# Performance work log

Measured on AMD Instinct MI355X. Metric: run time of the kernel, lower is better.

The kernel has to match this reference:

```python
import jax, jax.numpy as jnp
import numpy as np

HEADS = 16
HEAD_DIM = 128


def rotate_half(x):
    x1, x2 = x[..., : x.shape[-1] // 2], x[..., x.shape[-1] // 2 :]
    return jnp.concatenate((-x2, x1), axis=-1)


def setup_inputs() -> dict:
    key = jax.random.key(0)
    ks = jax.random.split(key, 8)
    b, s, h = 2, 2048, 2048
    d = HEAD_DIM
    sc = 1.0 / np.sqrt(h)
    x = jax.random.normal(ks[0], (b, s, h), jnp.float32)
    # real RoPE angles for realism
    inv_freq = 1.0 / (10000.0 ** (jnp.arange(0, d, 2, dtype=jnp.float32) / d))
    t = jnp.arange(s, dtype=jnp.float32)
    freqs = jnp.outer(t, inv_freq)  # [s, d/2]
    emb = jnp.concatenate((freqs, freqs), axis=-1)  # [s, d]
    return {
        "x": x,
        "cos": jnp.cos(emb),
        "sin": jnp.sin(emb),
        "wq": jax.random.normal(ks[1], (h, h), jnp.float32) * sc,
        "bq": jnp.zeros((h,), jnp.float32),
        "wk": jax.random.normal(ks[2], (h, h), jnp.float32) * sc,
        "bk": jnp.zeros((h,), jnp.float32),
        "wv": jax.random.normal(ks[3], (h, h), jnp.float32) * sc,
        "bv": jnp.zeros((h,), jnp.float32),
        "wo": jax.random.normal(ks[4], (h, h), jnp.float32) * sc,
    }


def reference(x, cos, sin, wq, bq, wk, bk, wv, bv, wo):
    b, s, hidden = x.shape
    nh, d = HEADS, HEAD_DIM
    # QKV projections (F.linear: x @ W.T + b)
    def split_heads(t):
        return t.reshape(b, s, nh, d).transpose(0, 2, 1, 3)  # [b,h,s,d]
    q = split_heads(x @ wq.T + bq)
    k = split_heads(x @ wk.T + bk)
    v = split_heads(x @ wv.T + bv)
    # RoPE (cos/sin: [s,d] broadcast over [b,h,s,d])
    q = q * cos + rotate_half(q) * sin
    k = k * cos + rotate_half(k) * sin
    # full (non-causal) attention, materializing [b,h,s,s] scores as original
    scale = 1.0 / jnp.sqrt(jnp.asarray(d, x.dtype))
    scores = jnp.einsum("bhqd,bhkd->bhqk", q, k) * scale
    attn = jax.nn.softmax(scores, axis=-1)
    out = jnp.einsum("bhqk,bhkd->bhqd", attn, v)  # [b,h,s,d]
    out = out.transpose(0, 2, 1, 3).reshape(b, s, hidden)
    # o_proj: no bias
    return out @ wo.T
```

## Files before the change

kernel.cpp:

```cpp
#include <hip/hip_runtime.h>

#define B_  2
#define NH  16
#define S_  2048
#define D_  128
#define HID 2048

typedef _Float16 half_t;
typedef _Float16 f16x8 __attribute__((ext_vector_type(8)));
typedef _Float16 f16x4_t __attribute__((ext_vector_type(4)));
typedef float f32x4 __attribute__((ext_vector_type(4)));

__device__ __forceinline__ void glds16(const half_t* g, half_t* l) {
    __builtin_amdgcn_global_load_lds(
        (const __attribute__((address_space(1))) void*)g,
        (__attribute__((address_space(3))) void*)l, 16, 0, 0);
}
__device__ __forceinline__ float fexp2(float x) { return __builtin_amdgcn_exp2f(x); }

__global__ __launch_bounds__(256) void cvt_all(
    const float* __restrict__ x,  const float* __restrict__ wq, const float* __restrict__ wk,
    const float* __restrict__ wv, const float* __restrict__ wo, half_t* __restrict__ dst)
{
    long i = ((long)blockIdx.x * 256 + threadIdx.x) * 4;
    const float* src; long off;
    if (i < 8388608)       { src = x;  off = i; }
    else if (i < 12582912) { src = wq; off = i - 8388608; }
    else if (i < 16777216) { src = wk; off = i - 12582912; }
    else if (i < 20971520) { src = wv; off = i - 16777216; }
    else                   { src = wo; off = i - 20971520; }
    float4 v = *(const float4*)(src + off);
    f16x4_t h;
    h[0] = (half_t)v.x; h[1] = (half_t)v.y; h[2] = (half_t)v.z; h[3] = (half_t)v.w;
    *(f16x4_t*)(dst + i) = h;
}

__global__ __launch_bounds__(256, 3) void qkv_gemm(
    const half_t* __restrict__ xb,
    const half_t* __restrict__ wqb, const half_t* __restrict__ wkb, const half_t* __restrict__ wvb,
    const float* __restrict__ bq, const float* __restrict__ bk, const float* __restrict__ bv,
    const float* __restrict__ cosp, const float* __restrict__ sinp,
    half_t* __restrict__ qo, half_t* __restrict__ ko, half_t* __restrict__ vto)
{
    __shared__ __align__(16) half_t As[128 * 32];
    __shared__ __align__(16) half_t Bs[128 * 32];
    const int m0 = blockIdx.x * 128;
    const int n0 = blockIdx.y * 128;
    const int z  = blockIdx.z;
    const half_t* wb   = (z == 0) ? wqb : (z == 1) ? wkb : wvb;
    const float*  bias = (z == 0) ? bq  : (z == 1) ? bk  : bv;
    const int tid = threadIdx.x, wave = tid >> 6, lane = tid & 63;
    const int quad = lane >> 4, lrow = lane & 15;
    const int wm = wave >> 1, wn = wave & 1;

    const int r0 = wave * 32 + (lane >> 2);
    const int r1 = r0 + 16;
    const int c0 = (((lane & 3) - (r0 >> 1)) & 3) * 8;
    const int c1 = (((lane & 3) - (r1 >> 1)) & 3) * 8;
    const half_t* ag0 = xb + (size_t)(m0 + r0) * HID + c0;
    const half_t* ag1 = xb + (size_t)(m0 + r1) * HID + c1;
    const half_t* bg0 = wb + (size_t)(n0 + r0) * HID + c0;
    const half_t* bg1 = wb + (size_t)(n0 + r1) * HID + c1;
    half_t* al0 = &As[(wave * 32) * 32];
    half_t* al1 = &As[(wave * 32 + 16) * 32];
    half_t* bl0 = &Bs[(wave * 32) * 32];
    half_t* bl1 = &Bs[(wave * 32 + 16) * 32];

    f32x4 acc[4][4] = {};

    for (int k0 = 0; k0 < HID; k0 += 32) {
        __syncthreads();
        glds16(ag0 + k0, al0);
        glds16(ag1 + k0, al1);
        glds16(bg0 + k0, bl0);
        glds16(bg1 + k0, bl1);
        __syncthreads();
        f16x8 af[4], bf[4];
#pragma unroll
        for (int mt = 0; mt < 4; mt++) {
            const int ra = wm * 64 + mt * 16 + lrow;
            const int pa = (quad + (ra >> 1)) & 3;
            af[mt] = *(const f16x8*)&As[ra * 32 + pa * 8];
        }
#pragma unroll
        for (int nt = 0; nt < 4; nt++) {
            const int rb = wn * 16 + nt * 32 + lrow;
            const int pb = (quad + (rb >> 1)) & 3;
            bf[nt] = *(const f16x8*)&Bs[rb * 32 + pb * 8];
        }
#pragma unroll
        for (int mt = 0; mt < 4; mt++)
#pragma unroll
            for (int nt = 0; nt < 4; nt++)
                acc[mt][nt] = __builtin_amdgcn_mfma_f32_16x16x32_f16(af[mt], bf[nt], acc[mt][nt], 0, 0, 0);
    }

    const int head = blockIdx.y;
    float bs_[4];
#pragma unroll
    for (int nt = 0; nt < 4; nt++) bs_[nt] = bias[n0 + nt * 32 + wn * 16 + lrow];
#pragma unroll
    for (int mt = 0; mt < 4; mt++) {
#pragma unroll
        for (int r = 0; r < 4; r++) {
            const int m  = m0 + wm * 64 + mt * 16 + quad * 4 + r;
            const int bb = m >> 11;
            const int st = m & (S_ - 1);
            float res[4];
#pragma unroll
            for (int nt = 0; nt < 4; nt++) res[nt] = acc[mt][nt][r] + bs_[nt];
            if (z < 2) {
                const float* cr = cosp + st * D_;
                const float* sr = sinp + st * D_;
#pragma unroll
                for (int pr = 0; pr < 2; pr++) {
                    const int dlo = pr * 32 + wn * 16 + lrow;
                    float cl = cr[dlo], sl = sr[dlo], ch = cr[dlo + 64], sh = sr[dlo + 64];
                    float lo = res[pr], hi = res[pr + 2];
                    res[pr]     = lo * cl - hi * sl;
                    res[pr + 2] = hi * ch + lo * sh;
                }
                half_t* dst = (z == 0 ? qo : ko) + ((size_t)(bb * NH + head) * S_ + st) * D_;
#pragma unroll
                for (int nt = 0; nt < 4; nt++) dst[nt * 32 + wn * 16 + lrow] = (half_t)res[nt];
            } else {
                half_t* dst = vto + (size_t)(bb * NH + head) * D_ * S_ + st;
#pragma unroll
                for (int nt = 0; nt < 4; nt++) dst[(size_t)(nt * 32 + wn * 16 + lrow) * S_] = (half_t)res[nt];
            }
        }
    }
}

#define PLD 72
__global__ __launch_bounds__(256, 2) void attn_kernel(
    const half_t* __restrict__ qb, const half_t* __restrict__ kb,
    const half_t* __restrict__ vtb, half_t* __restrict__ ob)
{
    __shared__ __align__(16) half_t ks[64 * 128];
    __shared__ __align__(16) half_t vs[128 * 64];
    __shared__ __align__(16) half_t ps[4 * 32 * PLD];
    const int head = blockIdx.y, b = blockIdx.z;
    const int bh = b * NH + head;
    const int tid = threadIdx.x, wave = tid >> 6, lane = tid & 63;
    const int quad = lane >> 4, lrow = lane & 15;
    const float SC = 0.08838834764831845f * 1.4426950408889634f;
    const int q0 = blockIdx.x * 128 + wave * 32;

    f16x8 qf[2][4];
#pragma unroll
    for (int mt = 0; mt < 2; mt++) {
        const half_t* qrow = qb + ((size_t)bh * S_ + q0 + mt * 16 + lrow) * D_;
#pragma unroll
        for (int kc = 0; kc < 4; kc++) {
            f16x8 v = *(const f16x8*)(qrow + kc * 32 + quad * 8);
#pragma unroll
            for (int j = 0; j < 8; j++) v[j] = (half_t)((float)v[j] * SC);
            qf[mt][kc] = v;
        }
    }

    const half_t* kbase = kb + (size_t)bh * S_ * D_;
    const half_t* vbase = vtb + (size_t)bh * D_ * S_;
    const int pbase = wave * 32 * PLD;

    float m_run[2] = {-1e30f, -1e30f}, l_run[2] = {0.f, 0.f};
    f32x4 o[2][8] = {};

    for (int kt = 0; kt < 32; kt++) {
        __syncthreads();
#pragma unroll
        for (int i = 0; i < 4; i++) {
            const int rk = wave * 16 + i * 4 + (lane >> 4);
            const int ck = (((lane & 15) - (rk & 7)) & 15) * 8;
            glds16(kbase + (size_t)(kt * 64 + rk) * D_ + ck, &ks[(wave * 16 + i * 4) * 128]);
            const int rv = wave * 32 + i * 8 + (lane >> 3);
            const int cv = (((lane & 7) - (rv & 7)) & 7) * 8;
            glds16(vbase + (size_t)rv * S_ + kt * 64 + cv, &vs[(wave * 32 + i * 8) * 64]);
        }
        __syncthreads();

        f32x4 st[2][4] = {};
#pragma unroll
        for (int nt = 0; nt < 4; nt++) {
            const int rk2 = nt * 16 + lrow;
#pragma unroll
            for (int kc = 0; kc < 4; kc++) {
                const int pk = (kc * 4 + quad + (rk2 & 7)) & 15;
                f16x8 kf = *(const f16x8*)&ks[rk2 * 128 + pk * 8];
                st[0][nt] = __builtin_amdgcn_mfma_f32_16x16x32_f16(kf, qf[0][kc], st[0][nt], 0, 0, 0);
                st[1][nt] = __builtin_amdgcn_mfma_f32_16x16x32_f16(kf, qf[1][kc], st[1][nt], 0, 0, 0);
            }
        }

        bool upd = false;
        float alpha[2];
#pragma unroll
        for (int mt = 0; mt < 2; mt++) {
            float m01 = fmaxf(fmaxf(st[mt][0][0], st[mt][0][1]), fmaxf(st[mt][0][2], st[mt][0][3]));
            float m11 = fmaxf(fmaxf(st[mt][1][0], st[mt][1][1]), fmaxf(st[mt][1][2], st[mt][1][3]));
            float m21 = fmaxf(fmaxf(st[mt][2][0], st[mt][2][1]), fmaxf(st[mt][2][2], st[mt][2][3]));
            float m31 = fmaxf(fmaxf(st[mt][3][0], st[mt][3][1]), fmaxf(st[mt][3][2], st[mt][3][3]));
            float mx = fmaxf(fmaxf(m01, m11), fmaxf(m21, m31));
            mx = fmaxf(mx, __shfl_xor(mx, 16));
            mx = fmaxf(mx, __shfl_xor(mx, 32));
            const float mnew = fmaxf(m_run[mt], mx);
            alpha[mt] = fexp2(m_run[mt] - mnew);
            upd = upd || (mnew > m_run[mt]);
            m_run[mt] = mnew;
            float rs = 0.f;
#pragma unroll
            for (int nt = 0; nt < 4; nt++) {
                f16x4_t pk4;
#pragma unroll
                for (int r = 0; r < 4; r++) {
                    float p = fexp2(st[mt][nt][r] - mnew);
                    rs += p;
                    pk4[r] = (half_t)p;
                }
                *(f16x4_t*)&ps[pbase + (mt * 16 + lrow) * PLD + nt * 16 + quad * 4] = pk4;
            }
            rs += __shfl_xor(rs, 16);
            rs += __shfl_xor(rs, 32);
            l_run[mt] = l_run[mt] * alpha[mt] + rs;
        }
        if (__any(upd)) {
#pragma unroll
            for (int mt = 0; mt < 2; mt++) {
                float ab[4];
#pragma unroll
                for (int r = 0; r < 4; r++) ab[r] = __shfl(alpha[mt], quad * 4 + r, 16);
#pragma unroll
                for (int dt = 0; dt < 8; dt++)
#pragma unroll
                    for (int r = 0; r < 4; r++) o[mt][dt][r] *= ab[r];
            }
        }

#pragma unroll
        for (int kc2 = 0; kc2 < 2; kc2++) {
            f16x8 pf0 = *(const f16x8*)&ps[pbase + lrow * PLD + kc2 * 32 + quad * 8];
            f16x8 pf1 = *(const f16x8*)&ps[pbase + (16 + lrow) * PLD + kc2 * 32 + quad * 8];
#pragma unroll
            for (int dt = 0; dt < 8; dt++) {
                const int rv2 = dt * 16 + lrow;
                const int pv = (kc2 * 4 + quad + (rv2 & 7)) & 7;
                f16x8 vf = *(const f16x8*)&vs[rv2 * 64 + pv * 8];
                o[0][dt] = __builtin_amdgcn_mfma_f32_16x16x32_f16(pf0, vf, o[0][dt], 0, 0, 0);
                o[1][dt] = __builtin_amdgcn_mfma_f32_16x16x32_f16(pf1, vf, o[1][dt], 0, 0, 0);
            }
        }
    }

#pragma unroll
    for (int mt = 0; mt < 2; mt++) {
        const float rl = 1.f / l_run[mt];
        float rb[4];
#pragma unroll
        for (int r = 0; r < 4; r++) rb[r] = __shfl(rl, quad * 4 + r, 16);
#pragma unroll
        for (int dt = 0; dt < 8; dt++) {
            const int d = dt * 16 + lrow;
#pragma unroll
            for (int r = 0; r < 4; r++) {
                const int row = q0 + mt * 16 + quad * 4 + r;
                ob[((size_t)b * S_ + row) * HID + head * D_ + d] = (half_t)(o[mt][dt][r] * rb[r]);
            }
        }
    }
}

__global__ __launch_bounds__(256, 3) void out_gemm(
    const half_t* __restrict__ ab, const half_t* __restrict__ wob, float* __restrict__ out)
{
    __shared__ __align__(16) half_t As[128 * 32];
    __shared__ __align__(16) half_t Bs[128 * 32];
    const int m0 = blockIdx.x * 128;
    const int n0 = blockIdx.y * 128;
    const int tid = threadIdx.x, wave = tid >> 6, lane = tid & 63;
    const int quad = lane >> 4, lrow = lane & 15;
    const int wm = wave >> 1, wn = wave & 1;

    const int r0 = wave * 32 + (lane >> 2);
    const int r1 = r0 + 16;
    const int c0 = (((lane & 3) - (r0 >> 1)) & 3) * 8;
    const int c1 = (((lane & 3) - (r1 >> 1)) & 3) * 8;
    const half_t* ag0 = ab  + (size_t)(m0 + r0) * HID + c0;
    const half_t* ag1 = ab  + (size_t)(m0 + r1) * HID + c1;
    const half_t* bg0 = wob + (size_t)(n0 + r0) * HID + c0;
    const half_t* bg1 = wob + (size_t)(n0 + r1) * HID + c1;
    half_t* al0 = &As[(wave * 32) * 32];
    half_t* al1 = &As[(wave * 32 + 16) * 32];
    half_t* bl0 = &Bs[(wave * 32) * 32];
    half_t* bl1 = &Bs[(wave * 32 + 16) * 32];

    f32x4 acc[4][4] = {};

    for (int k0 = 0; k0 < HID; k0 += 32) {
        __syncthreads();
        glds16(ag0 + k0, al0);
        glds16(ag1 + k0, al1);
        glds16(bg0 + k0, bl0);
        glds16(bg1 + k0, bl1);
        __syncthreads();
        f16x8 af[4], bf[4];
#pragma unroll
        for (int mt = 0; mt < 4; mt++) {
            const int ra = wm * 64 + mt * 16 + lrow;
            const int pa = (quad + (ra >> 1)) & 3;
            af[mt] = *(const f16x8*)&As[ra * 32 + pa * 8];
        }
#pragma unroll
        for (int nt = 0; nt < 4; nt++) {
            const int rb = wn * 16 + nt * 32 + lrow;
            const int pb = (quad + (rb >> 1)) & 3;
            bf[nt] = *(const f16x8*)&Bs[rb * 32 + pb * 8];
        }
#pragma unroll
        for (int mt = 0; mt < 4; mt++)
#pragma unroll
            for (int nt = 0; nt < 4; nt++)
                acc[mt][nt] = __builtin_amdgcn_mfma_f32_16x16x32_f16(af[mt], bf[nt], acc[mt][nt], 0, 0, 0);
    }

#pragma unroll
    for (int mt = 0; mt < 4; mt++)
#pragma unroll
        for (int r = 0; r < 4; r++) {
            const int m = m0 + wm * 64 + mt * 16 + quad * 4 + r;
#pragma unroll
            for (int nt = 0; nt < 4; nt++)
                out[(size_t)m * HID + n0 + nt * 32 + wn * 16 + lrow] = acc[mt][nt][r];
        }
}

extern "C" void kernel_launch(void* const* d_in, const int* in_sizes, int n_in,
                              void* d_out, int out_size, void* d_ws, size_t ws_size,
                              hipStream_t stream)
{
    const float* x    = (const float*)d_in[0];
    const float* cosp = (const float*)d_in[1];
    const float* sinp = (const float*)d_in[2];
    const float* wq   = (const float*)d_in[3];
    const float* bq   = (const float*)d_in[4];
    const float* wk   = (const float*)d_in[5];
    const float* bk   = (const float*)d_in[6];
    const float* wv   = (const float*)d_in[7];
    const float* bv   = (const float*)d_in[8];
    const float* wo   = (const float*)d_in[9];
    float* out = (float*)d_out;

    half_t* w   = (half_t*)d_ws;
    half_t* xb  = w;
    half_t* wqb = xb  + 8388608;
    half_t* wkb = wqb + 4194304;
    half_t* wvb = wkb + 4194304;
    half_t* wob = wvb + 4194304;
    half_t* qo  = wob + 4194304;
    half_t* ko  = qo  + 8388608;
    half_t* vto = ko  + 8388608;
    half_t* ob  = vto + 8388608;

    cvt_all<<<24576, 256, 0, stream>>>(x, wq, wk, wv, wo, xb);
    qkv_gemm<<<dim3(32, 16, 3), 256, 0, stream>>>(xb, wqb, wkb, wvb, bq, bk, bv,
                                                  cosp, sinp, qo, ko, vto);
    attn_kernel<<<dim3(16, 16, 2), 256, 0, stream>>>(qo, ko, vto, ob);
    out_gemm<<<dim3(32, 16), 256, 0, stream>>>(ob, wob, out);
}
```

Before: 422.4 us.

## Load GEMM and attention operands directly from global memory, dropping LDS staging

Removes the shared-memory staging (global_load_lds plus barriers) in the QKV GEMM, output GEMM and attention kernels. Each wave now loads its MFMA fragments straight from global memory into registers. The GEMMs double-buffer those register fragments to prefetch the next k-slice. The aim is to cut barrier and LDS traffic, but every wave now re-reads operands from global/L2 that were previously shared across the block, which raises memory traffic and register pressure.

```diff
diff --git a/kernel.cpp b/kernel.cpp
--- a/kernel.cpp
+++ b/kernel.cpp
@@ -11,11 +11,6 @@
 typedef _Float16 f16x4_t __attribute__((ext_vector_type(4)));
 typedef float f32x4 __attribute__((ext_vector_type(4)));
 
-__device__ __forceinline__ void glds16(const half_t* g, half_t* l) {
-    __builtin_amdgcn_global_load_lds(
-        (const __attribute__((address_space(1))) void*)g,
-        (__attribute__((address_space(3))) void*)l, 16, 0, 0);
-}
 __device__ __forceinline__ float fexp2(float x) { return __builtin_amdgcn_exp2f(x); }
 
 __global__ __launch_bounds__(256) void cvt_all(
@@ -42,8 +37,6 @@
     const float* __restrict__ cosp, const float* __restrict__ sinp,
     half_t* __restrict__ qo, half_t* __restrict__ ko, half_t* __restrict__ vto)
 {
-    __shared__ __align__(16) half_t As[128 * 32];
-    __shared__ __align__(16) half_t Bs[128 * 32];
     const int m0 = blockIdx.x * 128;
     const int n0 = blockIdx.y * 128;
     const int z  = blockIdx.z;
@@ -53,47 +46,37 @@
     const int quad = lane >> 4, lrow = lane & 15;
     const int wm = wave >> 1, wn = wave & 1;
 
-    const int r0 = wave * 32 + (lane >> 2);
-    const int r1 = r0 + 16;
-    const int c0 = (((lane & 3) - (r0 >> 1)) & 3) * 8;
-    const int c1 = (((lane & 3) - (r1 >> 1)) & 3) * 8;
-    const half_t* ag0 = xb + (size_t)(m0 + r0) * HID + c0;
-    const half_t* ag1 = xb + (size_t)(m0 + r1) * HID + c1;
-    const half_t* bg0 = wb + (size_t)(n0 + r0) * HID + c0;
-    const half_t* bg1 = wb + (size_t)(n0 + r1) * HID + c1;
-    half_t* al0 = &As[(wave * 32) * 32];
-    half_t* al1 = &As[(wave * 32 + 16) * 32];
-    half_t* bl0 = &Bs[(wave * 32) * 32];
-    half_t* bl1 = &Bs[(wave * 32 + 16) * 32];
-
+    const half_t* ap = xb + (size_t)(m0 + wm * 64 + lrow) * HID + quad * 8;
+    const half_t* bp = wb + (size_t)(n0 + wn * 16 + lrow) * HID + quad * 8;
+
+    f16x8 afr[2][4], bfr[2][4];
     f32x4 acc[4][4] = {};
 
-    for (int k0 = 0; k0 < HID; k0 += 32) {
-        __syncthreads();
-        glds16(ag0 + k0, al0);
-        glds16(ag1 + k0, al1);
-        glds16(bg0 + k0, bl0);
-        glds16(bg1 + k0, bl1);
-        __syncthreads();
-        f16x8 af[4], bf[4];
-#pragma unroll
-        for (int mt = 0; mt < 4; mt++) {
-            const int ra = wm * 64 + mt * 16 + lrow;
-            const int pa = (quad + (ra >> 1)) & 3;
-            af[mt] = *(const f16x8*)&As[ra * 32 + pa * 8];
-        }
-#pragma unroll
-        for (int nt = 0; nt < 4; nt++) {
-            const int rb = wn * 16 + nt * 32 + lrow;
-            const int pb = (quad + (rb >> 1)) & 3;
-            bf[nt] = *(const f16x8*)&Bs[rb * 32 + pb * 8];
-        }
+#pragma unroll
+    for (int mt = 0; mt < 4; mt++) afr[0][mt] = *(const f16x8*)(ap + (size_t)mt * 16 * HID);
+#pragma unroll
+    for (int nt = 0; nt < 4; nt++) bfr[0][nt] = *(const f16x8*)(bp + (size_t)nt * 32 * HID);
+
+#pragma unroll 2
+    for (int k0 = 0; k0 < HID - 32; k0 += 32) {
+        const int p = (k0 >> 5) & 1, pn = p ^ 1;
 #pragma unroll
         for (int mt = 0; mt < 4; mt++)
+            afr[pn][mt] = *(const f16x8*)(ap + k0 + 32 + (size_t)mt * 16 * HID);
+#pragma unroll
+        for (int nt = 0; nt < 4; nt++)
+            bfr[pn][nt] = *(const f16x8*)(bp + k0 + 32 + (size_t)nt * 32 * HID);
+#pragma unroll
+        for (int mt = 0; mt < 4; mt++)
 #pragma unroll
             for (int nt = 0; nt < 4; nt++)
-                acc[mt][nt] = __builtin_amdgcn_mfma_f32_16x16x32_f16(af[mt], bf[nt], acc[mt][nt], 0, 0, 0);
-    }
+                acc[mt][nt] = __builtin_amdgcn_mfma_f32_16x16x32_f16(afr[p][mt], bfr[p][nt], acc[mt][nt], 0, 0, 0);
+    }
+#pragma unroll
+    for (int mt = 0; mt < 4; mt++)
+#pragma unroll
+        for (int nt = 0; nt < 4; nt++)
+            acc[mt][nt] = __builtin_amdgcn_mfma_f32_16x16x32_f16(afr[1][mt], bfr[1][nt], acc[mt][nt], 0, 0, 0);
 
     const int head = blockIdx.y;
     float bs_[4];
@@ -137,8 +120,6 @@
     const half_t* __restrict__ qb, const half_t* __restrict__ kb,
     const half_t* __restrict__ vtb, half_t* __restrict__ ob)
 {
-    __shared__ __align__(16) half_t ks[64 * 128];
-    __shared__ __align__(16) half_t vs[128 * 64];
     __shared__ __align__(16) half_t ps[4 * 32 * PLD];
     const int head = blockIdx.y, b = blockIdx.z;
     const int bh = b * NH + head;
@@ -168,28 +149,17 @@
     f32x4 o[2][8] = {};
 
     for (int kt = 0; kt < 32; kt++) {
-        __syncthreads();
-#pragma unroll
-        for (int i = 0; i < 4; i++) {
-            const int rk = wave * 16 + i * 4 + (lane >> 4);
-            const int ck = (((lane & 15) - (rk & 7)) & 15) * 8;
-            glds16(kbase + (size_t)(kt * 64 + rk) * D_ + ck, &ks[(wave * 16 + i * 4) * 128]);
-            const int rv = wave * 32 + i * 8 + (lane >> 3);
-            const int cv = (((lane & 7) - (rv & 7)) & 7) * 8;
-            glds16(vbase + (size_t)rv * S_ + kt * 64 + cv, &vs[(wave * 32 + i * 8) * 64]);
-        }
-        __syncthreads();
-
         f32x4 st[2][4] = {};
 #pragma unroll
         for (int nt = 0; nt < 4; nt++) {
-            const int rk2 = nt * 16 + lrow;
+            const half_t* krow = kbase + (size_t)(kt * 64 + nt * 16 + lrow) * D_ + quad * 8;
+            f16x8 kf[4];
+#pragma unroll
+            for (int kc = 0; kc < 4; kc++) kf[kc] = *(const f16x8*)(krow + kc * 32);
 #pragma unroll
             for (int kc = 0; kc < 4; kc++) {
-                const int pk = (kc * 4 + quad + (rk2 & 7)) & 15;
-                f16x8 kf = *(const f16x8*)&ks[rk2 * 128 + pk * 8];
-                st[0][nt] = __builtin_amdgcn_mfma_f32_16x16x32_f16(kf, qf[0][kc], st[0][nt], 0, 0, 0);
-                st[1][nt] = __builtin_amdgcn_mfma_f32_16x16x32_f16(kf, qf[1][kc], st[1][nt], 0, 0, 0);
+                st[0][nt] = __builtin_amdgcn_mfma_f32_16x16x32_f16(kf[kc], qf[0][kc], st[0][nt], 0, 0, 0);
+                st[1][nt] = __builtin_amdgcn_mfma_f32_16x16x32_f16(kf[kc], qf[1][kc], st[1][nt], 0, 0, 0);
             }
         }
 
@@ -241,11 +211,10 @@
         for (int kc2 = 0; kc2 < 2; kc2++) {
             f16x8 pf0 = *(const f16x8*)&ps[pbase + lrow * PLD + kc2 * 32 + quad * 8];
             f16x8 pf1 = *(const f16x8*)&ps[pbase + (16 + lrow) * PLD + kc2 * 32 + quad * 8];
+            const half_t* vcol = vbase + kt * 64 + kc2 * 32 + quad * 8;
 #pragma unroll
             for (int dt = 0; dt < 8; dt++) {
-                const int rv2 = dt * 16 + lrow;
-                const int pv = (kc2 * 4 + quad + (rv2 & 7)) & 7;
-                f16x8 vf = *(const f16x8*)&vs[rv2 * 64 + pv * 8];
+                f16x8 vf = *(const f16x8*)(vcol + (size_t)(dt * 16 + lrow) * S_);
                 o[0][dt] = __builtin_amdgcn_mfma_f32_16x16x32_f16(pf0, vf, o[0][dt], 0, 0, 0);
                 o[1][dt] = __builtin_amdgcn_mfma_f32_16x16x32_f16(pf1, vf, o[1][dt], 0, 0, 0);
             }
@@ -273,55 +242,43 @@
 __global__ __launch_bounds__(256, 3) void out_gemm(
     const half_t* __restrict__ ab, const half_t* __restrict__ wob, float* __restrict__ out)
 {
-    __shared__ __align__(16) half_t As[128 * 32];
-    __shared__ __align__(16) half_t Bs[128 * 32];
     const int m0 = blockIdx.x * 128;
     const int n0 = blockIdx.y * 128;
     const int tid = threadIdx.x, wave = tid >> 6, lane = tid & 63;
     const int quad = lane >> 4, lrow = lane & 15;
     const int wm = wave >> 1, wn = wave & 1;
 
-    const int r0 = wave * 32 + (lane >> 2);
-    const int r1 = r0 + 16;
-    const int c0 = (((lane & 3) - (r0 >> 1)) & 3) * 8;
-    const int c1 = (((lane & 3) - (r1 >> 1)) & 3) * 8;
-    const half_t* ag0 = ab  + (size_t)(m0 + r0) * HID + c0;
-    const half_t* ag1 = ab  + (size_t)(m0 + r1) * HID + c1;
-    const half_t* bg0 = wob + (size_t)(n0 + r0) * HID + c0;
-    const half_t* bg1 = wob + (size_t)(n0 + r1) * HID + c1;
-    half_t* al0 = &As[(wave * 32) * 32];
-    half_t* al1 = &As[(wave * 32 + 16) * 32];
-    half_t* bl0 = &Bs[(wave * 32) * 32];
-    half_t* bl1 = &Bs[(wave * 32 + 16) * 32];
-
+    const half_t* ap = ab  + (size_t)(m0 + wm * 64 + lrow) * HID + quad * 8;
+    const half_t* bp = wob + (size_t)(n0 + wn * 16 + lrow) * HID + quad * 8;
+
+    f16x8 afr[2][4], bfr[2][4];
     f32x4 acc[4][4] = {};
 
-    for (int k0 = 0; k0 < HID; k0 += 32) {
-        __syncthreads();
-        glds16(ag0 + k0, al0);
-        glds16(ag1 + k0, al1);
-        glds16(bg0 + k0, bl0);
-        glds16(bg1 + k0, bl1);
-        __syncthreads();
-        f16x8 af[4], bf[4];
-#pragma unroll
-        for (int mt = 0; mt < 4; mt++) {
-            const int ra = wm * 64 + mt * 16 + lrow;
-            const int pa = (quad + (ra >> 1)) & 3;
-            af[mt] = *(const f16x8*)&As[ra * 32 + pa * 8];
-        }
-#pragma unroll
-        for (int nt = 0; nt < 4; nt++) {
-            const int rb = wn * 16 + nt * 32 + lrow;
-            const int pb = (quad + (rb >> 1)) & 3;
-            bf[nt] = *(const f16x8*)&Bs[rb * 32 + pb * 8];
-        }
+#pragma unroll
+    for (int mt = 0; mt < 4; mt++) afr[0][mt] = *(const f16x8*)(ap + (size_t)mt * 16 * HID);
+#pragma unroll
+    for (int nt = 0; nt < 4; nt++) bfr[0][nt] = *(const f16x8*)(bp + (size_t)nt * 32 * HID);
+
+#pragma unroll 2
+    for (int k0 = 0; k0 < HID - 32; k0 += 32) {
+        const int p = (k0 >> 5) & 1, pn = p ^ 1;
 #pragma unroll
         for (int mt = 0; mt < 4; mt++)
+            afr[pn][mt] = *(const f16x8*)(ap + k0 + 32 + (size_t)mt * 16 * HID);
+#pragma unroll
+        for (int nt = 0; nt < 4; nt++)
+            bfr[pn][nt] = *(const f16x8*)(bp + k0 + 32 + (size_t)nt * 32 * HID);
+#pragma unroll
+        for (int mt = 0; mt < 4; mt++)
 #pragma unroll
             for (int nt = 0; nt < 4; nt++)
-                acc[mt][nt] = __builtin_amdgcn_mfma_f32_16x16x32_f16(af[mt], bf[nt], acc[mt][nt], 0, 0, 0);
-    }
+                acc[mt][nt] = __builtin_amdgcn_mfma_f32_16x16x32_f16(afr[p][mt], bfr[p][nt], acc[mt][nt], 0, 0, 0);
+    }
+#pragma unroll
+    for (int mt = 0; mt < 4; mt++)
+#pragma unroll
+        for (int nt = 0; nt < 4; nt++)
+            acc[mt][nt] = __builtin_amdgcn_mfma_f32_16x16x32_f16(afr[1][mt], bfr[1][nt], acc[mt][nt], 0, 0, 0);
 
 #pragma unroll
     for (int mt = 0; mt < 4; mt++)
```

Result: slower. 887.3 us (+110.1%).
